# Kernel optimization log

Measured on AMD Instinct MI355X. Metric: run time of the kernel, lower is better.

Reference implementation:

```python
import jax, jax.numpy as jnp
import numpy as np

N = 8192       # subgraph nodes
F_IN = 512     # input feature dim
F_OUT = 256    # hidden dim (hardcoded 256 in fit())
M = 4096       # masked output nodes
DENSITY = 0.01
NEG_SLOPE = 0.01  # nn.LeakyReLU default


def setup_inputs() -> dict:
    key = jax.random.key(0)
    k_adj, k_feat, k_w, k_a1, k_a2, k_mask = jax.random.split(key, 6)
    adj = (jax.random.uniform(k_adj, (N, N)) < DENSITY).astype(jnp.float32)
    adj = jnp.maximum(adj, jnp.eye(N, dtype=jnp.float32))  # self-loops (sampler always adds them)
    eye = jnp.eye(N, dtype=jnp.float32)
    feats = jax.random.normal(k_feat, (N, F_IN), dtype=jnp.float32)
    W = jax.random.normal(k_w, (F_OUT, F_IN), dtype=jnp.float32) * (1.0 / np.sqrt(F_IN))
    b = jnp.zeros((F_OUT,), dtype=jnp.float32)
    a_1 = jax.random.uniform(k_a1, (1, F_OUT), dtype=jnp.float32)
    a_2 = jax.random.uniform(k_a2, (1, F_OUT), dtype=jnp.float32)
    node_mask = jax.random.randint(k_mask, (M,), 0, N)
    return {"adj_matrix": adj, "eye_matrix": eye, "subgraph_feats": feats,
            "node_mask": node_mask, "W": W, "b": b, "a_1": a_1, "a_2": a_2}


def reference(adj_matrix, eye_matrix, subgraph_feats, node_mask, W, b, a_1, a_2):
    z = subgraph_feats @ W.T + b                         # [N, F_OUT]
    zi = jnp.sum(a_1 * z, axis=1, keepdims=True)         # [N, 1]
    zj = jnp.sum(a_2 * z, axis=1, keepdims=True)         # [N, 1]
    att = adj_matrix * zi + adj_matrix * (eye_matrix * zj)  # [N, N]
    att = jnp.exp(jax.nn.leaky_relu(att, NEG_SLOPE)) * adj_matrix
    att = att / jnp.sum(att, axis=1, keepdims=True)      # row-normalize
    h = z - att @ z                                      # residual subtract aggregate
    return jax.nn.relu(h[node_mask])                     # [M, F_OUT]
```

## Files before the change

kernel.cpp:

```cpp
#include <hip/hip_runtime.h>
#include <hip/hip_bf16.h>


typedef float  f32x4  __attribute__((ext_vector_type(4)));
typedef short  s16x8  __attribute__((ext_vector_type(8)));
typedef unsigned short u16x4 __attribute__((ext_vector_type(4)));

#define KDIM  512
#define NODES 8192
#define FOUT  256
#define MOUT  4096

static __device__ inline unsigned short f2bf(float f) {
    union { float f; unsigned u; } x; x.f = f;
    unsigned r = x.u + 0x7FFFu + ((x.u >> 16) & 1u);
    return (unsigned short)(r >> 16);
}
static __device__ inline float bf2f(unsigned short u) {
    union { unsigned u; float f; } x; x.u = ((unsigned)u) << 16;
    return x.f;
}

__global__ __launch_bounds__(256) void gemm_z(
    const float* __restrict__ feats,
    const float* __restrict__ W,
    const float* __restrict__ bias,
    float* __restrict__ zf,
    unsigned short* __restrict__ zb)
{
    __shared__ unsigned short lA[128 * 32];
    __shared__ unsigned short lB[128 * 32];

    const int tid  = threadIdx.x;
    const int lane = tid & 63;
    const int wave = tid >> 6;
    const int quad = lane >> 4;
    const int l16  = lane & 15;
    const int bm = blockIdx.x;
    const int bn = blockIdx.y;
    const int wr = wave >> 1, wc = wave & 1;

    f32x4 acc[4][4] = {};

    const int r   = tid >> 1;
    const int seg = tid & 1;
    const float* gA = feats + (size_t)(bm * 128 + r) * KDIM + seg * 16;
    const float* gB = W     + (size_t)(bn * 128 + r) * KDIM + seg * 16;
    unsigned short* sA = &lA[r * 32 + seg * 16];
    unsigned short* sB = &lB[r * 32 + seg * 16];

    for (int kt = 0; kt < KDIM; kt += 32) {
        __syncthreads();
        f32x4 av[4], bv[4];
        #pragma unroll
        for (int i = 0; i < 4; i++) {
            av[i] = *(const f32x4*)(gA + kt + i * 4);
            bv[i] = *(const f32x4*)(gB + kt + i * 4);
        }
        s16x8 pa0, pa1, pb0, pb1;
        #pragma unroll
        for (int j = 0; j < 8; j++) {
            pa0[j] = (short)f2bf(av[j >> 2][j & 3]);
            pa1[j] = (short)f2bf(av[2 + (j >> 2)][j & 3]);
            pb0[j] = (short)f2bf(bv[j >> 2][j & 3]);
            pb1[j] = (short)f2bf(bv[2 + (j >> 2)][j & 3]);
        }
        ((s16x8*)sA)[0] = pa0; ((s16x8*)sA)[1] = pa1;
        ((s16x8*)sB)[0] = pb0; ((s16x8*)sB)[1] = pb1;
        __syncthreads();

        s16x8 af[4], bfr[4];
        #pragma unroll
        for (int mi = 0; mi < 4; mi++)
            af[mi] = *(const s16x8*)&lA[(wr * 64 + mi * 16 + l16) * 32 + quad * 8];
        #pragma unroll
        for (int ni = 0; ni < 4; ni++)
            bfr[ni] = *(const s16x8*)&lB[(wc * 64 + ni * 16 + l16) * 32 + quad * 8];
        #pragma unroll
        for (int mi = 0; mi < 4; mi++)
            #pragma unroll
            for (int ni = 0; ni < 4; ni++)
                acc[mi][ni] = __builtin_amdgcn_mfma_f32_16x16x32_bf16(
                    af[mi], bfr[ni], acc[mi][ni], 0, 0, 0);
    }

    #pragma unroll
    for (int ni = 0; ni < 4; ni++) {
        const int gcol = bn * 128 + wc * 64 + ni * 16 + l16;
        const float bv = bias[gcol];
        #pragma unroll
        for (int mi = 0; mi < 4; mi++) {
            const int grow0 = bm * 128 + wr * 64 + mi * 16 + quad * 4;
            #pragma unroll
            for (int rr = 0; rr < 4; rr++) {
                const float v = acc[mi][ni][rr] + bv;
                const size_t off = (size_t)(grow0 + rr) * FOUT + gcol;
                zf[off] = v;
                zb[off] = f2bf(v);
            }
        }
    }
}

__global__ __launch_bounds__(256) void attn_rows(
    const float* __restrict__ adj,
    const int*   __restrict__ mask,
    const float* __restrict__ zf,
    const unsigned short* __restrict__ zb,
    const float* __restrict__ a1,
    const float* __restrict__ a2,
    float* __restrict__ out)
{
    const int lane = threadIdx.x & 63;
    const int wave = threadIdx.x >> 6;
    const int m = blockIdx.x * 4 + wave;
    const int row = mask[m];

    const f32x4 zr  = *(const f32x4*)(zf + (size_t)row * FOUT + 4 * lane);
    const f32x4 va1 = *(const f32x4*)(a1 + 4 * lane);
    const f32x4 va2 = *(const f32x4*)(a2 + 4 * lane);

    float zi = va1[0] * zr[0] + va1[1] * zr[1] + va1[2] * zr[2] + va1[3] * zr[3];
    float zj = va2[0] * zr[0] + va2[1] * zr[1] + va2[2] * zr[2] + va2[3] * zr[3];
    #pragma unroll
    for (int off = 32; off; off >>= 1) {
        zi += __shfl_xor(zi, off);
        zj += __shfl_xor(zj, off);
    }

    f32x4 S = {0.f, 0.f, 0.f, 0.f};
    int deg = 0;
    const float* arow = adj + (size_t)row * NODES;
    for (int chunk = 0; chunk < NODES; chunk += 256) {
        const f32x4 v = *(const f32x4*)(arow + chunk + 4 * lane);
        #pragma unroll
        for (int t = 0; t < 4; t++) {
            unsigned long long mk = __ballot(v[t] != 0.0f);
            deg += __popcll(mk);
            while (mk) {
                const int s = __builtin_ctzll(mk);
                mk &= mk - 1;
                const int j = chunk + 4 * s + t;
                const u16x4 zn = *(const u16x4*)(zb + (size_t)j * FOUT + 4 * lane);
                S[0] += bf2f(zn[0]);
                S[1] += bf2f(zn[1]);
                S[2] += bf2f(zn[2]);
                S[3] += bf2f(zn[3]);
            }
        }
    }

    const float li = zi > 0.f ? zi : 0.01f * zi;
    const float sd = zi + zj;
    const float ld = sd > 0.f ? sd : 0.01f * sd;
    const float e_off  = expf(li);
    const float e_diag = expf(ld);
    const float denom  = (float)(deg - 1) * e_off + e_diag;
    const float w_off  = e_off / denom;
    const float w_d    = e_diag / denom;
    const float coef   = 1.0f + w_off - w_d;

    f32x4 h;
    #pragma unroll
    for (int t = 0; t < 4; t++) {
        const float hv = zr[t] * coef - w_off * S[t];
        h[t] = hv > 0.f ? hv : 0.f;
    }
    *(f32x4*)(out + (size_t)m * FOUT + 4 * lane) = h;
}

extern "C" void kernel_launch(void* const* d_in, const int* in_sizes, int n_in,
                              void* d_out, int out_size, void* d_ws, size_t ws_size,
                              hipStream_t stream)
{
    const float* adj   = (const float*)d_in[0];
    const float* feats = (const float*)d_in[2];
    const int*   mask  = (const int*)d_in[3];
    const float* W     = (const float*)d_in[4];
    const float* bias  = (const float*)d_in[5];
    const float* a1    = (const float*)d_in[6];
    const float* a2    = (const float*)d_in[7];
    float* out = (float*)d_out;

    float* zf = (float*)d_ws;
    unsigned short* zb = (unsigned short*)((char*)d_ws + (size_t)NODES * FOUT * 4);

    dim3 g1(NODES / 128, FOUT / 128);
    gemm_z<<<g1, dim3(256), 0, stream>>>(feats, W, bias, zf, zb);
    attn_rows<<<dim3(MOUT / 4), dim3(256), 0, stream>>>(adj, mask, zf, zb, a1, a2, out);
}
```

Before: 500.5 us.

## Pre-convert GEMM inputs to bf16, use direct-to-LDS loads, split attention row across block

```diff
diff --git a/kernel.cpp b/kernel.cpp
--- a/kernel.cpp
+++ b/kernel.cpp
@@ -21,9 +21,34 @@
     return x.f;
 }
 
+static __device__ inline void gload_lds16(const void* g, void* l) {
+    __builtin_amdgcn_global_load_lds(
+        (const __attribute__((address_space(1))) unsigned int*)g,
+        (__attribute__((address_space(3))) unsigned int*)l, 16, 0, 0);
+}
+
+#define FEAT_G (NODES * KDIM / 8)
+#define W_G    (FOUT * KDIM / 8)
+__global__ __launch_bounds__(256) void to_bf16(
+    const float* __restrict__ feats, const float* __restrict__ W,
+    unsigned short* __restrict__ fb, unsigned short* __restrict__ wb)
+{
+    const int t = blockIdx.x * 256 + threadIdx.x;
+    const float* src;
+    unsigned short* dst;
+    if (t < FEAT_G) { src = feats + (size_t)t * 8; dst = fb + (size_t)t * 8; }
+    else           { const int u = t - FEAT_G; src = W + (size_t)u * 8; dst = wb + (size_t)u * 8; }
+    const f32x4 a = *(const f32x4*)src;
+    const f32x4 b = *(const f32x4*)(src + 4);
+    s16x8 p;
+    #pragma unroll
+    for (int j = 0; j < 4; j++) { p[j] = (short)f2bf(a[j]); p[4 + j] = (short)f2bf(b[j]); }
+    *(s16x8*)dst = p;
+}
+
 __global__ __launch_bounds__(256) void gemm_z(
-    const float* __restrict__ feats,
-    const float* __restrict__ W,
+    const unsigned short* __restrict__ fb,
+    const unsigned short* __restrict__ wb,
     const float* __restrict__ bias,
     float* __restrict__ zf,
     unsigned short* __restrict__ zb)
@@ -42,31 +67,19 @@
 
     f32x4 acc[4][4] = {};
 
-    const int r   = tid >> 1;
-    const int seg = tid & 1;
-    const float* gA = feats + (size_t)(bm * 128 + r) * KDIM + seg * 16;
-    const float* gB = W     + (size_t)(bn * 128 + r) * KDIM + seg * 16;
-    unsigned short* sA = &lA[r * 32 + seg * 16];
-    unsigned short* sB = &lB[r * 32 + seg * 16];
+    const int rowA = tid >> 2;
+    const int c8   = tid & 3;
+    const unsigned short* gA = fb + (size_t)(bm * 128 + rowA) * KDIM + c8 * 8;
+    const unsigned short* gB = wb + (size_t)(bn * 128 + rowA) * KDIM + c8 * 8;
+    char* dA = (char*)lA + tid * 16;
+    char* dB = (char*)lB + tid * 16;
 
     for (int kt = 0; kt < KDIM; kt += 32) {
         __syncthreads();
-        f32x4 av[4], bv[4];
-        #pragma unroll
-        for (int i = 0; i < 4; i++) {
-            av[i] = *(const f32x4*)(gA + kt + i * 4);
-            bv[i] = *(const f32x4*)(gB + kt + i * 4);
-        }
-        s16x8 pa0, pa1, pb0, pb1;
-        #pragma unroll
-        for (int j = 0; j < 8; j++) {
-            pa0[j] = (short)f2bf(av[j >> 2][j & 3]);
-            pa1[j] = (short)f2bf(av[2 + (j >> 2)][j & 3]);
-            pb0[j] = (short)f2bf(bv[j >> 2][j & 3]);
-            pb1[j] = (short)f2bf(bv[2 + (j >> 2)][j & 3]);
-        }
-        ((s16x8*)sA)[0] = pa0; ((s16x8*)sA)[1] = pa1;
-        ((s16x8*)sB)[0] = pb0; ((s16x8*)sB)[1] = pb1;
+        gload_lds16(gA + kt,            dA);
+        gload_lds16(gA + kt + 64 * KDIM, dA + 4096);
+        gload_lds16(gB + kt,            dB);
+        gload_lds16(gB + kt + 64 * KDIM, dB + 4096);
         __syncthreads();
 
         s16x8 af[4], bfr[4];
@@ -102,6 +115,8 @@
     }
 }
 
+#define IDX_CAP 512
+
 __global__ __launch_bounds__(256) void attn_rows(
     const float* __restrict__ adj,
     const int*   __restrict__ mask,
@@ -111,62 +126,105 @@
     const float* __restrict__ a2,
     float* __restrict__ out)
 {
-    const int lane = threadIdx.x & 63;
-    const int wave = threadIdx.x >> 6;
-    const int m = blockIdx.x * 4 + wave;
-    const int row = mask[m];
-
-    const f32x4 zr  = *(const f32x4*)(zf + (size_t)row * FOUT + 4 * lane);
-    const f32x4 va1 = *(const f32x4*)(a1 + 4 * lane);
-    const f32x4 va2 = *(const f32x4*)(a2 + 4 * lane);
-
-    float zi = va1[0] * zr[0] + va1[1] * zr[1] + va1[2] * zr[2] + va1[3] * zr[3];
-    float zj = va2[0] * zr[0] + va2[1] * zr[1] + va2[2] * zr[2] + va2[3] * zr[3];
+    __shared__ int   s_idx[4][IDX_CAP];
+    __shared__ int   s_cnt[4];
+    __shared__ float s_red[2][4];
+    __shared__ float s_S[4][FOUT];
+
+    const int tid  = threadIdx.x;
+    const int lane = tid & 63;
+    const int wave = tid >> 6;
+    const int m    = blockIdx.x;
+    const int row  = mask[m];
+
+    const float zt = zf[(size_t)row * FOUT + tid];
+    float p1 = a1[tid] * zt;
+    float p2 = a2[tid] * zt;
     #pragma unroll
     for (int off = 32; off; off >>= 1) {
-        zi += __shfl_xor(zi, off);
-        zj += __shfl_xor(zj, off);
-    }
+        p1 += __shfl_xor(p1, off);
+        p2 += __shfl_xor(p2, off);
+    }
+    if (lane == 0) { s_red[0][wave] = p1; s_red[1][wave] = p2; }
+
+    int cnt = 0;
+    const float* arow = adj + (size_t)row * NODES + wave * 2048;
+    #pragma unroll
+    for (int c = 0; c < 2048; c += 256) {
+        const f32x4 v = *(const f32x4*)(arow + c + 4 * lane);
+        #pragma unroll
+        for (int t = 0; t < 4; t++) {
+            const bool nz = (v[t] != 0.0f);
+            const unsigned long long mk = __ballot(nz);
+            const int pre = __popcll(mk & ((1ull << lane) - 1ull));
+            if (nz) {
+                const int slot = cnt + pre;
+                if (slot < IDX_CAP)
+                    s_idx[wave][slot] = wave * 2048 + c + 4 * lane + t;
+            }
+            cnt += __popcll(mk);
+        }
+    }
+    if (lane == 0) s_cnt[wave] = cnt;
+    __syncthreads();
+
+    const int deg = s_cnt[0] + s_cnt[1] + s_cnt[2] + s_cnt[3];
 
     f32x4 S = {0.f, 0.f, 0.f, 0.f};
-    int deg = 0;
-    const float* arow = adj + (size_t)row * NODES;
-    for (int chunk = 0; chunk < NODES; chunk += 256) {
-        const f32x4 v = *(const f32x4*)(arow + chunk + 4 * lane);
+    const int myc = s_cnt[wave];
+    int i = 0;
+    for (; i + 4 <= myc; i += 4) {
+        const int j0 = s_idx[wave][i + 0];
+        const int j1 = s_idx[wave][i + 1];
+        const int j2 = s_idx[wave][i + 2];
+        const int j3 = s_idx[wave][i + 3];
+        const u16x4 z0 = *(const u16x4*)(zb + (size_t)j0 * FOUT + 4 * lane);
+        const u16x4 z1 = *(const u16x4*)(zb + (size_t)j1 * FOUT + 4 * lane);
+        const u16x4 z2 = *(const u16x4*)(zb + (size_t)j2 * FOUT + 4 * lane);
+        const u16x4 z3 = *(const u16x4*)(zb + (size_t)j3 * FOUT + 4 * lane);
+        #pragma unroll
+        for (int t = 0; t < 4; t++)
+            S[t] += bf2f(z0[t]) + bf2f(z1[t]) + bf2f(z2[t]) + bf2f(z3[t]);
+    }
+    for (; i < myc; i++) {
+        const int j = s_idx[wave][i];
+        const u16x4 zn = *(const u16x4*)(zb + (size_t)j * FOUT + 4 * lane);
+        #pragma unroll
+        for (int t = 0; t < 4; t++) S[t] += bf2f(zn[t]);
+    }
+    *(f32x4*)&s_S[wave][4 * lane] = S;
+    __syncthreads();
+
+    if (wave == 0) {
+        f32x4 St = *(const f32x4*)&s_S[0][4 * lane];
+        #pragma unroll
+        for (int w = 1; w < 4; w++) {
+            const f32x4 Sw = *(const f32x4*)&s_S[w][4 * lane];
+            #pragma unroll
+            for (int t = 0; t < 4; t++) St[t] += Sw[t];
+        }
+        const float zi = s_red[0][0] + s_red[0][1] + s_red[0][2] + s_red[0][3];
+        const float zj = s_red[1][0] + s_red[1][1] + s_red[1][2] + s_red[1][3];
+
+        const float li = zi > 0.f ? zi : 0.01f * zi;
+        const float sd = zi + zj;
+        const float ld = sd > 0.f ? sd : 0.01f * sd;
+        const float e_off  = expf(li);
+        const float e_diag = expf(ld);
+        const float denom  = (float)(deg - 1) * e_off + e_diag;
+        const float w_off  = e_off / denom;
+        const float w_d    = e_diag / denom;
+        const float coef   = 1.0f + w_off - w_d;
+
+        const f32x4 zr = *(const f32x4*)(zf + (size_t)row * FOUT + 4 * lane);
+        f32x4 h;
         #pragma unroll
         for (int t = 0; t < 4; t++) {
-            unsigned long long mk = __ballot(v[t] != 0.0f);
-            deg += __popcll(mk);
-            while (mk) {
-                const int s = __builtin_ctzll(mk);
-                mk &= mk - 1;
-                const int j = chunk + 4 * s + t;
-                const u16x4 zn = *(const u16x4*)(zb + (size_t)j * FOUT + 4 * lane);
-                S[0] += bf2f(zn[0]);
-                S[1] += bf2f(zn[1]);
-                S[2] += bf2f(zn[2]);
-                S[3] += bf2f(zn[3]);
-            }
-        }
-    }
-
-    const float li = zi > 0.f ? zi : 0.01f * zi;
-    const float sd = zi + zj;
-    const float ld = sd > 0.f ? sd : 0.01f * sd;
-    const float e_off  = expf(li);
-    const float e_diag = expf(ld);
-    const float denom  = (float)(deg - 1) * e_off + e_diag;
-    const float w_off  = e_off / denom;
-    const float w_d    = e_diag / denom;
-    const float coef   = 1.0f + w_off - w_d;
-
-    f32x4 h;
-    #pragma unroll
-    for (int t = 0; t < 4; t++) {
-        const float hv = zr[t] * coef - w_off * S[t];
-        h[t] = hv > 0.f ? hv : 0.f;
-    }
-    *(f32x4*)(out + (size_t)m * FOUT + 4 * lane) = h;
+            const float hv = zr[t] * coef - w_off * St[t];
+            h[t] = hv > 0.f ? hv : 0.f;
+        }
+        *(f32x4*)(out + (size_t)m * FOUT + 4 * lane) = h;
+    }
 }
 
 extern "C" void kernel_launch(void* const* d_in, const int* in_sizes, int n_in,
@@ -182,10 +240,13 @@
     const float* a2    = (const float*)d_in[7];
     float* out = (float*)d_out;
 
-    float* zf = (float*)d_ws;
-    unsigned short* zb = (unsigned short*)((char*)d_ws + (size_t)NODES * FOUT * 4);
-
-    dim3 g1(NODES / 128, FOUT / 128);
-    gemm_z<<<g1, dim3(256), 0, stream>>>(feats, W, bias, zf, zb);
-    attn_rows<<<dim3(MOUT / 4), dim3(256), 0, stream>>>(adj, mask, zf, zb, a1, a2, out);
-}
+    char* ws = (char*)d_ws;
+    float*          zf = (float*)          (ws);
+    unsigned short* zb = (unsigned short*) (ws + 8388608);
+    unsigned short* fb = (unsigned short*) (ws + 12582912);
+    unsigned short* wb = (unsigned short*) (ws + 20971520);
+
+    to_bf16<<<dim3((FEAT_G + W_G) / 256), dim3(256), 0, stream>>>(feats, W, fb, wb);
+    gemm_z<<<dim3(NODES / 128, FOUT / 128), dim3(256), 0, stream>>>(fb, wb, bias, zf, zb);
+    attn_rows<<<dim3(MOUT), dim3(256), 0, stream>>>(adj, mask, zf, zb, a1, a2, out);
+}
```

Measured after the change: 470.4 us. -6.0%, faster.
